# Kernel tuning notes

Measured on AMD Instinct MI355X. Metric: run time of the kernel, lower is better.

Reference implementation:

```python
import jax, jax.numpy as jnp
from jax import lax
import numpy as np

B, L, N_NODES, EMB, TDIM, H, NCLS = 512, 200, 100000, 128, 10, 256, 2
IN = TDIM + EMB  # 138


def setup_inputs() -> dict:
    key = jax.random.key(0)
    ks = jax.random.split(key, 16)
    x = jax.random.randint(ks[0], (B, L, 2), 0, N_NODES, dtype=jnp.int64)
    s = 0.05
    inp = {
        'x': x,
        'emb_table': jax.random.normal(ks[1], (N_NODES, EMB), jnp.float32) * s,
        'ts_W': jnp.ones((1, TDIM), jnp.float32),
        'w_ih_f': jax.random.normal(ks[2], (4 * H, IN), jnp.float32) * s,
        'w_hh_f': jax.random.normal(ks[3], (4 * H, H), jnp.float32) * s,
        'b_ih_f': jax.random.normal(ks[4], (4 * H,), jnp.float32) * s,
        'b_hh_f': jax.random.normal(ks[5], (4 * H,), jnp.float32) * s,
        'w_ih_b': jax.random.normal(ks[6], (4 * H, IN), jnp.float32) * s,
        'w_hh_b': jax.random.normal(ks[7], (4 * H, H), jnp.float32) * s,
        'b_ih_b': jax.random.normal(ks[8], (4 * H,), jnp.float32) * s,
        'b_hh_b': jax.random.normal(ks[9], (4 * H,), jnp.float32) * s,
        'fc_W': jax.random.normal(ks[10], (NCLS, 2 * H), jnp.float32) * s,
        'fc_b': jax.random.normal(ks[11], (NCLS,), jnp.float32) * s,
    }
    return inp


def _lstm_dir(x_seq, w_ih, w_hh, b_ih, b_hh, reverse):
    # x_seq: [B, L, F]; PyTorch gate order i, f, g, o
    bsz = x_seq.shape[0]
    h_dim = w_hh.shape[1]
    xg = jnp.einsum('blf,gf->blg', x_seq, w_ih) + b_ih + b_hh  # [B, L, 4H]
    xs = jnp.swapaxes(xg, 0, 1)  # [L, B, 4H]
    if reverse:
        xs = xs[::-1]

    def step(carry, xg_t):
        h, c = carry
        g = xg_t + h @ w_hh.T
        i, f, gg, o = jnp.split(g, 4, axis=-1)
        c = jax.nn.sigmoid(f) * c + jax.nn.sigmoid(i) * jnp.tanh(gg)
        h = jax.nn.sigmoid(o) * jnp.tanh(c)
        return (h, c), h

    z = jnp.zeros((bsz, h_dim), x_seq.dtype)
    _, hs = lax.scan(step, (z, z), xs)
    hs = jnp.swapaxes(hs, 0, 1)  # [B, L, H]
    if reverse:
        hs = hs[:, ::-1]
    return hs


def reference(x, emb_table, ts_W, w_ih_f, w_hh_f, b_ih_f, b_hh_f,
              w_ih_b, w_hh_b, b_ih_b, b_hh_b, fc_W, fc_b):
    # timestamp embedding: [B, L, 1] @ [1, 10] -> [B, L, 10]
    t = x[:, :, 0:1].astype(jnp.float32)
    t_emb = t @ ts_W
    # F.normalize(p=2, dim=1): L2-normalize over the sequence axis
    norm = jnp.sqrt(jnp.sum(t_emb * t_emb, axis=1, keepdims=True))
    t_emb = t_emb / jnp.maximum(norm, 1e-12)

    # vectorized node-embedding gather; id == -1 -> zero vector
    ids = x[:, :, 1]
    gathered = emb_table[jnp.clip(ids, 0, None)]  # [B, L, 128]
    l_emb = jnp.where((ids >= 0)[..., None], gathered, jnp.zeros((), gathered.dtype))

    embedding = jnp.concatenate([t_emb, l_emb], axis=2)  # [B, L, 138]

    h_f = _lstm_dir(embedding, w_ih_f, w_hh_f, b_ih_f, b_hh_f, reverse=False)
    h_b = _lstm_dir(embedding, w_ih_b, w_hh_b, b_ih_b, b_hh_b, reverse=True)
    out = jnp.concatenate([h_f, h_b], axis=-1)  # [B, L, 2H]

    return out[:, -1, :] @ fc_W.T + fc_b  # [B, num_classes]
```

## Files before the change

kernel.cpp:

```cpp
#include <hip/hip_runtime.h>
#include <stdint.h>


typedef unsigned short u16;
typedef __bf16 bf16x8 __attribute__((ext_vector_type(8)));
typedef float  f32x4  __attribute__((ext_vector_type(4)));

#define B_    512
#define L_    200
#define EMB_  128
#define TDIM_ 10
#define IN_   138
#define INP_  160
#define H_    256
#define G4_   1024
#define T_    200
#define DS_   (1.0f/1024.0f)
#define LOG2E 1.4426950408889634f
#define EXP2(x) __builtin_amdgcn_exp2f(x)

static __device__ __forceinline__ float bf2f(u16 u) {
  union { uint32_t i; float f; } v; v.i = ((uint32_t)u) << 16; return v.f;
}
static __device__ __forceinline__ u16 f2bf(float f) {
  __bf16 h = (__bf16)f; return __builtin_bit_cast(u16, h);
}
static __device__ __forceinline__ float bflo(uint32_t u) {
  return __builtin_bit_cast(float, (uint32_t)(u << 16));
}
static __device__ __forceinline__ float bfhi(uint32_t u) {
  return __builtin_bit_cast(float, (uint32_t)(u & 0xffff0000u));
}
static __device__ __forceinline__ float sigf(float x) {
  return __builtin_amdgcn_rcpf(1.0f + EXP2(-x * LOG2E));
}
static __device__ __forceinline__ float tanh_(float x) {
  x = fminf(fmaxf(x, -15.f), 15.f);
  float e = EXP2(2.0f * LOG2E * x);
  return (e - 1.0f) * __builtin_amdgcn_rcpf(e + 1.0f);
}
static __device__ __forceinline__ f32x4 mfma16(bf16x8 a, bf16x8 b, f32x4 c) {
  return __builtin_amdgcn_mfma_f32_16x16x32_bf16(a, b, c, 0, 0, 0);
}
static __device__ __forceinline__ f32x4 vzero4() {
  f32x4 v; v[0] = 0.f; v[1] = 0.f; v[2] = 0.f; v[3] = 0.f; return v;
}

__global__ void k_norm(const int* __restrict__ x, float* __restrict__ s) {
  int b = blockIdx.x;
  int tid = threadIdx.x;
  float v = 0.f;
  if (tid < L_) {
    float t = (float)x[(b * L_ + tid) * 2];
    v = t * t;
  }
  #pragma unroll
  for (int o = 32; o; o >>= 1) v += __shfl_down(v, o);
  __shared__ float p[4];
  if ((tid & 63) == 0) p[tid >> 6] = v;
  __syncthreads();
  if (tid == 0) s[b] = p[0] + p[1] + p[2] + p[3];
}

__global__ void k_prep_w8(const float* __restrict__ whh, int* __restrict__ wf8) {
  int idx = blockIdx.x * blockDim.x + threadIdx.x;
  int jq = idx & 1;
  int lane = (idx >> 1) & 63;
  int fid = idx >> 7;
  int kp = fid & 7, tt = (fid >> 3) & 7, w = fid >> 6;
  int mm = lane & 15, q = lane >> 4;
  int g = (w + 8 * tt) * 16 + mm;
  int k = kp * 32 + q * 8 + jq * 4;
  const float* src = whh + g * 256 + k;
  int d = __builtin_amdgcn_cvt_pk_fp8_f32(src[0] * 64.f, src[1] * 64.f, 0, false);
  d     = __builtin_amdgcn_cvt_pk_fp8_f32(src[2] * 64.f, src[3] * 64.f, d, true);
  wf8[idx] = d;
}

__global__ void k_feat(const int* __restrict__ x, const float* __restrict__ emb,
                       const float* __restrict__ tsW, const float* __restrict__ s,
                       u16* __restrict__ feat) {
  int idx = blockIdx.x * blockDim.x + threadIdx.x;
  if (idx >= B_ * L_ * INP_) return;
  int c = idx % INP_;
  int row = idx / INP_;
  int b = row / L_;
  float v = 0.f;
  if (c < TDIM_) {
    float t = (float)x[row * 2 + 0];
    float wd = tsW[c];
    float den = fmaxf(fabsf(wd) * sqrtf(s[b]), 1e-12f);
    v = t * wd / den;
  } else if (c < IN_) {
    int id = x[row * 2 + 1];
    int idc = id < 0 ? 0 : id;
    float e = emb[(long)idc * EMB_ + (c - TDIM_)];
    v = (id >= 0) ? e : 0.f;
  }
  feat[idx] = f2bf(v);
}

__global__ __launch_bounds__(512) void k_xg(
    const u16* __restrict__ feat, const float* __restrict__ wih,
    const float* __restrict__ bih, const float* __restrict__ bhh,
    u16* __restrict__ xg) {
  __shared__ u16 Bs[256 * 176];
  const int nt = blockIdx.x;
  const int mt = blockIdx.y;
  const int tid = threadIdx.x;
  const int w = tid >> 6, lane = tid & 63;
  const int q = lane >> 4, nm = lane & 15;
  for (int i2 = tid; i2 < 256 * 88; i2 += 512) {
    int gl = i2 / 88, f2 = (i2 % 88) * 2;
    int pk = 0;
    if (f2 < IN_) {
      float2 v = *(const float2*)(wih + (long)(nt * 256 + gl) * IN_ + f2);
      pk = (int)f2bf(v.x) | ((int)f2bf(v.y) << 16);
    }
    *(int*)&Bs[gl * 176 + f2] = pk;
  }
  float bias[16];
  #pragma unroll
  for (int nu = 0; nu < 16; ++nu) {
    int g = nt * 256 + nu * 16 + nm;
    bias[nu] = bih[g] + bhh[g];
  }
  __syncthreads();
  f32x4 acc[16];
  #pragma unroll
  for (int nu = 0; nu < 16; ++nu) acc[nu] = vzero4();
  const u16* arow = feat + (long)(mt * 128 + w * 16) * INP_;
  #pragma unroll
  for (int kp = 0; kp < 5; ++kp) {
    bf16x8 a = *(const bf16x8*)(arow + (nm * INP_ + kp * 32 + q * 8));
    #pragma unroll
    for (int nu = 0; nu < 16; ++nu) {
      bf16x8 bb = *(const bf16x8*)&Bs[(nu * 16 + nm) * 176 + kp * 32 + q * 8];
      acc[nu] = mfma16(a, bb, acc[nu]);
    }
  }
  __syncthreads();
  u16* Os = Bs;
  #pragma unroll
  for (int nu = 0; nu < 16; ++nu) {
    #pragma unroll
    for (int r = 0; r < 4; ++r) {
      int row = w * 16 + 4 * q + r;
      Os[row * 264 + nu * 16 + nm] = f2bf((acc[nu][r] + bias[nu]) * 1024.f);
    }
  }
  __syncthreads();
  #pragma unroll
  for (int it = 0; it < 8; ++it) {
    int flat = it * 512 + tid;
    int row = flat >> 5, c = flat & 31;
    uint4 v = *(const uint4*)&Os[row * 264 + c * 8];
    *(uint4*)&xg[(long)(mt * 128 + row) * G4_ + nt * 256 + c * 8] = v;
  }
}

#define F8(A, B, C) __builtin_amdgcn_mfma_f32_16x16x32_fp8_fp8((A), (B), (C), 0, 0, 0)
#define WLD(tt) \
  long w##tt##_0 = wp[((tt) * 8 + 0) * 64]; \
  long w##tt##_1 = wp[((tt) * 8 + 1) * 64]; \
  long w##tt##_2 = wp[((tt) * 8 + 2) * 64]; \
  long w##tt##_3 = wp[((tt) * 8 + 3) * 64]; \
  long w##tt##_4 = wp[((tt) * 8 + 4) * 64]; \
  long w##tt##_5 = wp[((tt) * 8 + 5) * 64];
#define MK(kp) { \
  long bh = *(const long*)&hr[hbase + (kp) * 8]; \
  acc0 = F8(w0_##kp, bh, acc0); acc1 = F8(w1_##kp, bh, acc1); \
  acc2 = F8(w2_##kp, bh, acc2); acc3 = F8(w3_##kp, bh, acc3); \
  acc4 = F8(w4_##kp, bh, acc4); acc5 = F8(w5_##kp, bh, acc5); \
  acc6 = F8(w6_##kp, bh, acc6); acc7 = F8(w7_##kp, bh, acc7); }
#define MKL(slot, kp) { \
  long bh = *(const long*)&hr[hbase + (kp) * 8]; \
  const long* lw = ldsW + (w * 16 + (slot) * 8) * 64 + lane; \
  acc0 = F8(lw[0 * 64], bh, acc0); acc1 = F8(lw[1 * 64], bh, acc1); \
  acc2 = F8(lw[2 * 64], bh, acc2); acc3 = F8(lw[3 * 64], bh, acc3); \
  acc4 = F8(lw[4 * 64], bh, acc4); acc5 = F8(lw[5 * 64], bh, acc5); \
  acc6 = F8(lw[6 * 64], bh, acc6); acc7 = F8(lw[7 * 64], bh, acc7); }
#define AINIT(i) \
  f32x4 acc##i; acc##i[0] = bflo(pf##i.x); acc##i[1] = bfhi(pf##i.x); \
  acc##i[2] = bflo(pf##i.y); acc##i[3] = bfhi(pf##i.y);
#define PFL(i) pf##i = *(const uint2*)(xn + ((w + 8 * (i)) * 16 + 4 * q));
#define EPI(jj, aI, aF, aG, aO, cs) { \
  f32x4 hv; \
  _Pragma("unroll") \
  for (int r = 0; r < 4; ++r) { \
    float si = __builtin_amdgcn_rcpf(1.f + EXP2(aI[r] * c_sig)); \
    float sf = __builtin_amdgcn_rcpf(1.f + EXP2(aF[r] * c_sig)); \
    float so = __builtin_amdgcn_rcpf(1.f + EXP2(aO[r] * c_sig)); \
    float tg = 1.f - 2.f * __builtin_amdgcn_rcpf(1.f + EXP2(aG[r] * c_tg)); \
    float c = sf * cs[r] + si * tg; \
    float tc = 1.f - 2.f * __builtin_amdgcn_rcpf(1.f + EXP2(c * c_tc)); \
    cs[r] = c; hv[r] = so * tc; \
  } \
  int pk = __builtin_amdgcn_cvt_pk_fp8_f32(hv[0] * 16.f, hv[1] * 16.f, 0, false); \
  pk     = __builtin_amdgcn_cvt_pk_fp8_f32(hv[2] * 16.f, hv[3] * 16.f, pk, true); \
  hw[nn * 66 + 4 * w + 32 * (jj) + q] = pk; \
  if (t == T_ - 1) *(f32x4*)&hf[(long)b * H_ + 16 * w + 128 * (jj) + 4 * q] = hv; }

__global__ __launch_bounds__(512, 2) void k_lstm_f(
    const long* __restrict__ wf8, const u16* __restrict__ xg,
    float* __restrict__ hf) {
  __shared__ long ldsW[128 * 64];
  __shared__ int hls[2][16 * 66];
  const int tid = threadIdx.x;
  const int w = tid >> 6;
  const int lane = tid & 63;
  const int q = lane >> 4;
  const int nn = lane & 15;
  const int b = blockIdx.x * 16 + nn;
  const int hbase = nn * 66 + (q << 1);
  const float c_sig = -DS_ * LOG2E;
  const float c_tg  = 2.f * DS_ * LOG2E;
  const float c_tc  = 2.f * LOG2E;

  const long* wp = wf8 + (long)(w * 64) * 64 + lane;
  WLD(0) WLD(1) WLD(2) WLD(3) WLD(4) WLD(5) WLD(6) WLD(7)
  #pragma unroll
  for (int tt = 0; tt < 8; ++tt) {
    ldsW[(w * 16 + tt) * 64 + lane]     = wp[(tt * 8 + 6) * 64];
    ldsW[(w * 16 + 8 + tt) * 64 + lane] = wp[(tt * 8 + 7) * 64];
  }
  for (int i = tid; i < 16 * 66; i += 512) hls[0][i] = 0;

  const u16* xgb = xg + (long)b * (L_ * G4_);
  uint2 pf0, pf1, pf2, pf3, pf4, pf5, pf6, pf7;
  {
    const u16* xn = xgb;
    PFL(0) PFL(1) PFL(2) PFL(3) PFL(4) PFL(5) PFL(6) PFL(7)
  }
  f32x4 cst0 = vzero4(), cst1 = vzero4();
  __syncthreads();

  #pragma unroll 1
  for (int t = 0; t < T_; ++t) {
    asm volatile("" :
      "+v"(w0_0), "+v"(w0_1), "+v"(w0_2), "+v"(w0_3), "+v"(w0_4), "+v"(w0_5),
      "+v"(w1_0), "+v"(w1_1), "+v"(w1_2), "+v"(w1_3), "+v"(w1_4), "+v"(w1_5),
      "+v"(w2_0), "+v"(w2_1), "+v"(w2_2), "+v"(w2_3), "+v"(w2_4), "+v"(w2_5),
      "+v"(w3_0), "+v"(w3_1), "+v"(w3_2), "+v"(w3_3), "+v"(w3_4), "+v"(w3_5),
      "+v"(w4_0), "+v"(w4_1), "+v"(w4_2), "+v"(w4_3), "+v"(w4_4), "+v"(w4_5),
      "+v"(w5_0), "+v"(w5_1), "+v"(w5_2), "+v"(w5_3), "+v"(w5_4), "+v"(w5_5),
      "+v"(w6_0), "+v"(w6_1), "+v"(w6_2), "+v"(w6_3), "+v"(w6_4), "+v"(w6_5),
      "+v"(w7_0), "+v"(w7_1), "+v"(w7_2), "+v"(w7_3), "+v"(w7_4), "+v"(w7_5));
    AINIT(0) AINIT(1) AINIT(2) AINIT(3) AINIT(4) AINIT(5) AINIT(6) AINIT(7)
    {
      const u16* xn = xgb + (long)(t + 1 < T_ ? t + 1 : t) * G4_;
      PFL(0) PFL(1) PFL(2) PFL(3) PFL(4) PFL(5) PFL(6) PFL(7)
    }
    const int* hr = hls[t & 1];
    MKL(0, 6) MKL(1, 7)
    MK(0) MK(1) MK(2) MK(3) MK(4) MK(5)
    int* hw = hls[1 - (t & 1)];
    EPI(0, acc0, acc2, acc4, acc6, cst0)
    EPI(1, acc1, acc3, acc5, acc7, cst1)
    __asm__ volatile("" ::: "memory");
    __builtin_amdgcn_s_waitcnt(0xc07f);
    __builtin_amdgcn_s_barrier();
    __asm__ volatile("" ::: "memory");
  }
}

__global__ __launch_bounds__(256) void k_bwd(
    const u16* __restrict__ feat, const float* __restrict__ wih,
    const float* __restrict__ bih, const float* __restrict__ bhh,
    float* __restrict__ hb) {
  const int b0 = blockIdx.x * 8;
  const int tid = threadIdx.x;
  __shared__ float fv[8][IN_];
  for (int i = tid; i < 8 * IN_; i += 256) {
    int r = i / IN_, c = i % IN_;
    fv[r][c] = bf2f(feat[((long)(b0 + r) * L_ + (L_ - 1)) * INP_ + c]);
  }
  __syncthreads();
  float gi[8], gg[8], go[8];
  float bi_ = bih[tid] + bhh[tid];
  float bg_ = bih[2 * H_ + tid] + bhh[2 * H_ + tid];
  float bo_ = bih[3 * H_ + tid] + bhh[3 * H_ + tid];
  #pragma unroll
  for (int r = 0; r < 8; ++r) { gi[r] = bi_; gg[r] = bg_; go[r] = bo_; }
  const float* wi_ = wih + (long)tid * IN_;
  const float* wg_ = wih + (long)(2 * H_ + tid) * IN_;
  const float* wo_ = wih + (long)(3 * H_ + tid) * IN_;
  for (int f = 0; f < IN_; ++f) {
    float a = wi_[f], gc = wg_[f], oc = wo_[f];
    #pragma unroll
    for (int r = 0; r < 8; ++r) {
      float x = fv[r][f];
      gi[r] += a * x;
      gg[r] += gc * x;
      go[r] += oc * x;
    }
  }
  #pragma unroll
  for (int r = 0; r < 8; ++r) {
    float c = sigf(gi[r]) * tanh_(gg[r]);
    hb[(long)(b0 + r) * H_ + tid] = sigf(go[r]) * tanh_(c);
  }
}

__global__ void k_fc(const float* __restrict__ hf, const float* __restrict__ hb,
                     const float* __restrict__ fcw, const float* __restrict__ fcb,
                     float* __restrict__ out) {
  int b = blockIdx.x;
  int lane = threadIdx.x;
  float p0 = 0.f, p1 = 0.f;
  #pragma unroll
  for (int k = lane; k < 2 * H_; k += 64) {
    float v = (k < H_) ? hf[b * H_ + k] : hb[b * H_ + (k - H_)];
    p0 += v * fcw[k];
    p1 += v * fcw[2 * H_ + k];
  }
  #pragma unroll
  for (int o = 32; o; o >>= 1) {
    p0 += __shfl_down(p0, o);
    p1 += __shfl_down(p1, o);
  }
  if (lane == 0) {
    out[b * 2 + 0] = p0 + fcb[0];
    out[b * 2 + 1] = p1 + fcb[1];
  }
}

extern "C" void kernel_launch(void* const* d_in, const int* in_sizes, int n_in,
                              void* d_out, int out_size, void* d_ws, size_t ws_size,
                              hipStream_t stream) {
  const int*   x    = (const int*)  d_in[0];
  const float* emb  = (const float*)d_in[1];
  const float* tsW  = (const float*)d_in[2];
  const float* wihf = (const float*)d_in[3];
  const float* whhf = (const float*)d_in[4];
  const float* bihf = (const float*)d_in[5];
  const float* bhhf = (const float*)d_in[6];
  const float* wihb = (const float*)d_in[7];
  const float* bihb = (const float*)d_in[9];
  const float* bhhb = (const float*)d_in[10];
  const float* fcw  = (const float*)d_in[11];
  const float* fcb  = (const float*)d_in[12];
  float* out = (float*)d_out;

  char* ws = (char*)d_ws;
  float* s    = (float*)(ws);
  int*   wf8  = (int*)  (ws + 2048);
  u16*   feat = (u16*)  (ws + 264192);
  u16*   xg   = (u16*)  (ws + 33032192);
  float* hf   = (float*)(ws + 242747392);
  float* hb   = (float*)(ws + 243271680);

  k_norm   <<<dim3(512),     dim3(256), 0, stream>>>(x, s);
  k_prep_w8<<<dim3(256),     dim3(256), 0, stream>>>(whhf, wf8);
  k_feat   <<<dim3(64000),   dim3(256), 0, stream>>>(x, emb, tsW, s, feat);
  k_xg     <<<dim3(4, 800),  dim3(512), 0, stream>>>(feat, wihf, bihf, bhhf, xg);
  k_lstm_f <<<dim3(32),      dim3(512), 0, stream>>>((const long*)wf8, xg, hf);
  k_bwd    <<<dim3(64),      dim3(256), 0, stream>>>(feat, wihb, bihb, bhhb, hb);
  k_fc     <<<dim3(512),     dim3(64),  0, stream>>>(hf, hb, fcw, fcb, out);
}
```

Before: 884.6 us.

## Use 16x16x128 FP8 MFMA for LSTM recurrent matmul with repacked weights

Replaces the chain of 16x16x32 FP8 MFMAs in the forward LSTM recurrence with the wider 16x16x128 f8f6f4 MFMA via inline asm, cutting the instruction count per step by four. The recurrent weights are repacked into 32-byte fragments, half kept in registers and half split across two LDS arrays. The hidden-state LDS row stride becomes 68 so each lane can do vector loads. Manual s_nop padding is added to cover the asm MFMA result hazards, which risks wrong results or stalls if the hazard timing is off.

```diff
diff --git a/kernel.cpp b/kernel.cpp
--- a/kernel.cpp
+++ b/kernel.cpp
@@ -5,6 +5,8 @@
 typedef unsigned short u16;
 typedef __bf16 bf16x8 __attribute__((ext_vector_type(8)));
 typedef float  f32x4  __attribute__((ext_vector_type(4)));
+typedef int    i32x4v __attribute__((ext_vector_type(4)));
+typedef int    i32x8v __attribute__((ext_vector_type(8)));
 
 #define B_    512
 #define L_    200
@@ -62,19 +64,19 @@
   if (tid == 0) s[b] = p[0] + p[1] + p[2] + p[3];
 }
 
-__global__ void k_prep_w8(const float* __restrict__ whh, int* __restrict__ wf8) {
+__global__ void k_prep_mx(const float* __restrict__ whh, int* __restrict__ wf8) {
   int idx = blockIdx.x * blockDim.x + threadIdx.x;
-  int jq = idx & 1;
-  int lane = (idx >> 1) & 63;
-  int fid = idx >> 7;
-  int kp = fid & 7, tt = (fid >> 3) & 7, w = fid >> 6;
+  int d = idx & 7;
+  int lane = (idx >> 3) & 63;
+  int fs = idx >> 9;
+  int kp2 = fs & 1, tt = (fs >> 1) & 7, w = fs >> 4;
   int mm = lane & 15, q = lane >> 4;
   int g = (w + 8 * tt) * 16 + mm;
-  int k = kp * 32 + q * 8 + jq * 4;
+  int k = kp2 * 128 + q * 32 + d * 4;
   const float* src = whh + g * 256 + k;
-  int d = __builtin_amdgcn_cvt_pk_fp8_f32(src[0] * 64.f, src[1] * 64.f, 0, false);
-  d     = __builtin_amdgcn_cvt_pk_fp8_f32(src[2] * 64.f, src[3] * 64.f, d, true);
-  wf8[idx] = d;
+  int v = __builtin_amdgcn_cvt_pk_fp8_f32(src[0] * 64.f, src[1] * 64.f, 0, false);
+  v     = __builtin_amdgcn_cvt_pk_fp8_f32(src[2] * 64.f, src[3] * 64.f, v, true);
+  wf8[idx] = v;
 }
 
 __global__ void k_feat(const int* __restrict__ x, const float* __restrict__ emb,
@@ -159,31 +161,17 @@
   }
 }
 
-#define F8(A, B, C) __builtin_amdgcn_mfma_f32_16x16x32_fp8_fp8((A), (B), (C), 0, 0, 0)
-#define WLD(tt) \
-  long w##tt##_0 = wp[((tt) * 8 + 0) * 64]; \
-  long w##tt##_1 = wp[((tt) * 8 + 1) * 64]; \
-  long w##tt##_2 = wp[((tt) * 8 + 2) * 64]; \
-  long w##tt##_3 = wp[((tt) * 8 + 3) * 64]; \
-  long w##tt##_4 = wp[((tt) * 8 + 4) * 64]; \
-  long w##tt##_5 = wp[((tt) * 8 + 5) * 64];
-#define MK(kp) { \
-  long bh = *(const long*)&hr[hbase + (kp) * 8]; \
-  acc0 = F8(w0_##kp, bh, acc0); acc1 = F8(w1_##kp, bh, acc1); \
-  acc2 = F8(w2_##kp, bh, acc2); acc3 = F8(w3_##kp, bh, acc3); \
-  acc4 = F8(w4_##kp, bh, acc4); acc5 = F8(w5_##kp, bh, acc5); \
-  acc6 = F8(w6_##kp, bh, acc6); acc7 = F8(w7_##kp, bh, acc7); }
-#define MKL(slot, kp) { \
-  long bh = *(const long*)&hr[hbase + (kp) * 8]; \
-  const long* lw = ldsW + (w * 16 + (slot) * 8) * 64 + lane; \
-  acc0 = F8(lw[0 * 64], bh, acc0); acc1 = F8(lw[1 * 64], bh, acc1); \
-  acc2 = F8(lw[2 * 64], bh, acc2); acc3 = F8(lw[3 * 64], bh, acc3); \
-  acc4 = F8(lw[4 * 64], bh, acc4); acc5 = F8(lw[5 * 64], bh, acc5); \
-  acc6 = F8(lw[6 * 64], bh, acc6); acc7 = F8(lw[7 * 64], bh, acc7); }
+#define MX2(accv, A0, A1, B0, B1) \
+  asm volatile("v_mfma_f32_16x16x128_f8f6f4 %0, %1, %3, %0\n\t" \
+               "v_mfma_f32_16x16x128_f8f6f4 %0, %2, %4, %0" \
+               : "+v"(accv) : "v"(A0), "v"(A1), "v"(B0), "v"(B1));
 #define AINIT(i) \
   f32x4 acc##i; acc##i[0] = bflo(pf##i.x); acc##i[1] = bfhi(pf##i.x); \
   acc##i[2] = bflo(pf##i.y); acc##i[3] = bfhi(pf##i.y);
 #define PFL(i) pf##i = *(const uint2*)(xn + ((w + 8 * (i)) * 16 + 4 * q));
+#define ALDS(f) __builtin_shufflevector(ldsX[(w * 8 + (f)) * 64 + lane], \
+                                        ldsY[(w * 8 + (f)) * 64 + lane], \
+                                        0, 1, 2, 3, 4, 5, 6, 7)
 #define EPI(jj, aI, aF, aG, aO, cs) { \
   f32x4 hv; \
   _Pragma("unroll") \
@@ -198,33 +186,35 @@
   } \
   int pk = __builtin_amdgcn_cvt_pk_fp8_f32(hv[0] * 16.f, hv[1] * 16.f, 0, false); \
   pk     = __builtin_amdgcn_cvt_pk_fp8_f32(hv[2] * 16.f, hv[3] * 16.f, pk, true); \
-  hw[nn * 66 + 4 * w + 32 * (jj) + q] = pk; \
+  hw[nn * 68 + 4 * w + 32 * (jj) + q] = pk; \
   if (t == T_ - 1) *(f32x4*)&hf[(long)b * H_ + 16 * w + 128 * (jj) + 4 * q] = hv; }
 
 __global__ __launch_bounds__(512, 2) void k_lstm_f(
-    const long* __restrict__ wf8, const u16* __restrict__ xg,
+    const int* __restrict__ wf8, const u16* __restrict__ xg,
     float* __restrict__ hf) {
-  __shared__ long ldsW[128 * 64];
-  __shared__ int hls[2][16 * 66];
+  __shared__ i32x4v ldsX[64 * 64];
+  __shared__ i32x4v ldsY[64 * 64];
+  __shared__ int hls[2][16 * 68];
   const int tid = threadIdx.x;
   const int w = tid >> 6;
   const int lane = tid & 63;
   const int q = lane >> 4;
   const int nn = lane & 15;
   const int b = blockIdx.x * 16 + nn;
-  const int hbase = nn * 66 + (q << 1);
   const float c_sig = -DS_ * LOG2E;
   const float c_tg  = 2.f * DS_ * LOG2E;
   const float c_tc  = 2.f * LOG2E;
 
-  const long* wp = wf8 + (long)(w * 64) * 64 + lane;
-  WLD(0) WLD(1) WLD(2) WLD(3) WLD(4) WLD(5) WLD(6) WLD(7)
-  #pragma unroll
-  for (int tt = 0; tt < 8; ++tt) {
-    ldsW[(w * 16 + tt) * 64 + lane]     = wp[(tt * 8 + 6) * 64];
-    ldsW[(w * 16 + 8 + tt) * 64 + lane] = wp[(tt * 8 + 7) * 64];
-  }
-  for (int i = tid; i < 16 * 66; i += 512) hls[0][i] = 0;
+#define WREG(fi) (*(const i32x8v*)(wf8 + (long)((w * 16 + (fi)) * 64 + lane) * 8))
+  i32x8v W40 = WREG(8),  W41 = WREG(9),  W50 = WREG(10), W51 = WREG(11);
+  i32x8v W60 = WREG(12), W61 = WREG(13), W70 = WREG(14), W71 = WREG(15);
+  #pragma unroll
+  for (int f = 0; f < 8; ++f) {
+    i32x8v v = WREG(f);
+    ldsX[(w * 8 + f) * 64 + lane] = __builtin_shufflevector(v, v, 0, 1, 2, 3);
+    ldsY[(w * 8 + f) * 64 + lane] = __builtin_shufflevector(v, v, 4, 5, 6, 7);
+  }
+  for (int i = tid; i < 16 * 68; i += 512) hls[0][i] = 0;
 
   const u16* xgb = xg + (long)b * (L_ * G4_);
   uint2 pf0, pf1, pf2, pf3, pf4, pf5, pf6, pf7;
@@ -237,23 +227,31 @@
 
   #pragma unroll 1
   for (int t = 0; t < T_; ++t) {
-    asm volatile("" :
-      "+v"(w0_0), "+v"(w0_1), "+v"(w0_2), "+v"(w0_3), "+v"(w0_4), "+v"(w0_5),
-      "+v"(w1_0), "+v"(w1_1), "+v"(w1_2), "+v"(w1_3), "+v"(w1_4), "+v"(w1_5),
-      "+v"(w2_0), "+v"(w2_1), "+v"(w2_2), "+v"(w2_3), "+v"(w2_4), "+v"(w2_5),
-      "+v"(w3_0), "+v"(w3_1), "+v"(w3_2), "+v"(w3_3), "+v"(w3_4), "+v"(w3_5),
-      "+v"(w4_0), "+v"(w4_1), "+v"(w4_2), "+v"(w4_3), "+v"(w4_4), "+v"(w4_5),
-      "+v"(w5_0), "+v"(w5_1), "+v"(w5_2), "+v"(w5_3), "+v"(w5_4), "+v"(w5_5),
-      "+v"(w6_0), "+v"(w6_1), "+v"(w6_2), "+v"(w6_3), "+v"(w6_4), "+v"(w6_5),
-      "+v"(w7_0), "+v"(w7_1), "+v"(w7_2), "+v"(w7_3), "+v"(w7_4), "+v"(w7_5));
     AINIT(0) AINIT(1) AINIT(2) AINIT(3) AINIT(4) AINIT(5) AINIT(6) AINIT(7)
     {
       const u16* xn = xgb + (long)(t + 1 < T_ ? t + 1 : t) * G4_;
       PFL(0) PFL(1) PFL(2) PFL(3) PFL(4) PFL(5) PFL(6) PFL(7)
     }
     const int* hr = hls[t & 1];
-    MKL(0, 6) MKL(1, 7)
-    MK(0) MK(1) MK(2) MK(3) MK(4) MK(5)
+    i32x8v B0 = __builtin_shufflevector(
+        *(const i32x4v*)&hr[nn * 68 + q * 8],
+        *(const i32x4v*)&hr[nn * 68 + q * 8 + 4], 0, 1, 2, 3, 4, 5, 6, 7);
+    i32x8v B1 = __builtin_shufflevector(
+        *(const i32x4v*)&hr[nn * 68 + 32 + q * 8],
+        *(const i32x4v*)&hr[nn * 68 + 32 + q * 8 + 4], 0, 1, 2, 3, 4, 5, 6, 7);
+    {
+      i32x8v A0, A1;
+      A0 = ALDS(0); A1 = ALDS(1); MX2(acc0, A0, A1, B0, B1);
+      A0 = ALDS(2); A1 = ALDS(3); MX2(acc1, A0, A1, B0, B1);
+      A0 = ALDS(4); A1 = ALDS(5); MX2(acc2, A0, A1, B0, B1);
+      A0 = ALDS(6); A1 = ALDS(7); MX2(acc3, A0, A1, B0, B1);
+    }
+    MX2(acc4, W40, W41, B0, B1);
+    MX2(acc5, W50, W51, B0, B1);
+    MX2(acc6, W60, W61, B0, B1);
+    MX2(acc7, W70, W71, B0, B1);
+    asm volatile("s_nop 7\n\ts_nop 7"
+                 : "+v"(acc4), "+v"(acc5), "+v"(acc6), "+v"(acc7));
     int* hw = hls[1 - (t & 1)];
     EPI(0, acc0, acc2, acc4, acc6, cst0)
     EPI(1, acc1, acc3, acc5, acc7, cst1)
@@ -351,10 +349,10 @@
   float* hb   = (float*)(ws + 243271680);
 
   k_norm   <<<dim3(512),     dim3(256), 0, stream>>>(x, s);
-  k_prep_w8<<<dim3(256),     dim3(256), 0, stream>>>(whhf, wf8);
+  k_prep_mx<<<dim3(256),     dim3(256), 0, stream>>>(whhf, wf8);
   k_feat   <<<dim3(64000),   dim3(256), 0, stream>>>(x, emb, tsW, s, feat);
   k_xg     <<<dim3(4, 800),  dim3(512), 0, stream>>>(feat, wihf, bihf, bhhf, xg);
-  k_lstm_f <<<dim3(32),      dim3(512), 0, stream>>>((const long*)wf8, xg, hf);
+  k_lstm_f <<<dim3(32),      dim3(512), 0, stream>>>(wf8, xg, hf);
   k_bwd    <<<dim3(64),      dim3(256), 0, stream>>>(feat, wihb, bihb, bhhb, hb);
   k_fc     <<<dim3(512),     dim3(64),  0, stream>>>(hf, hb, fcw, fcb, out);
 }
```

Measured after the change: 804.3 us. 1.1x faster.
